# Performance work log

Measured on AMD Instinct MI355X. Metric: run time of the kernel, lower is better.

## Reference

```python
import jax, jax.numpy as jnp
import numpy as np

N_NODES = 50000
N_EDGES = 800000
N_GRAPHS = 64
IN_C = 64
HID = 64
HEADS = 4
NEG_SLOPE = 0.2
EPS = 1e-16


def setup_inputs() -> dict:
    key = jax.random.key(0)
    ks = jax.random.split(key, 16)
    x = jax.random.normal(ks[0], (N_NODES, IN_C), dtype=jnp.float32)
    edge_index = jax.random.randint(ks[1], (2, N_EDGES), 0, N_NODES, dtype=jnp.int64)
    batch = jnp.sort(jax.random.randint(ks[2], (N_NODES,), 0, N_GRAPHS, dtype=jnp.int64))
    s = 1.0 / np.sqrt(IN_C)
    s2 = 1.0 / np.sqrt(HID * HEADS)
    s3 = 1.0 / np.sqrt(HID)
    return {
        "x": x,
        "edge_index": edge_index,
        "batch": batch,
        # GATv2 layer 1: in 64 -> heads*64 = 256 (concat)
        "Wl1": jax.random.normal(ks[3], (IN_C, HEADS * HID), dtype=jnp.float32) * s,
        "Wr1": jax.random.normal(ks[4], (IN_C, HEADS * HID), dtype=jnp.float32) * s,
        "att1": jax.random.normal(ks[5], (HEADS, HID), dtype=jnp.float32) * s3,
        "b1": jnp.zeros((HEADS * HID,), dtype=jnp.float32),
        # GATv2 layer 2: in 256 -> 1 head * 64
        "Wl2": jax.random.normal(ks[6], (HEADS * HID, HID), dtype=jnp.float32) * s2,
        "Wr2": jax.random.normal(ks[7], (HEADS * HID, HID), dtype=jnp.float32) * s2,
        "att2": jax.random.normal(ks[8], (1, HID), dtype=jnp.float32) * s3,
        "b2": jnp.zeros((HID,), dtype=jnp.float32),
        # MLP head: 64 -> 64 -> 2
        "W3": jax.random.normal(ks[9], (HID, 64), dtype=jnp.float32) * s3,
        "b3": jnp.zeros((64,), dtype=jnp.float32),
        "W4": jax.random.normal(ks[10], (64, 2), dtype=jnp.float32) * (1.0 / 8.0),
        "b4": jnp.zeros((2,), dtype=jnp.float32),
    }


def gatv2_conv(x, src, dst, Wl, Wr, att, bias, heads, out_c, n_nodes):
    # PyG GATv2Conv (eval mode, add_self_loops=False, concat heads):
    # x_l = lin_l(x) used for SOURCE nodes (messages), x_r = lin_r(x) for TARGET nodes.
    xl = (x @ Wl).reshape(n_nodes, heads, out_c)
    xr = (x @ Wr).reshape(n_nodes, heads, out_c)
    e = jax.nn.leaky_relu(xl[src] + xr[dst], NEG_SLOPE)          # [E, H, C]
    logits = jnp.einsum('ehc,hc->eh', e, att)                    # [E, H]
    # numerically stable softmax over incoming edges of each target node
    m = jax.ops.segment_max(logits, dst, num_segments=n_nodes)   # [N, H]
    ex = jnp.exp(logits - m[dst])
    denom = jax.ops.segment_sum(ex, dst, num_segments=n_nodes)   # [N, H]
    alpha = ex / (denom[dst] + EPS)                              # [E, H]
    out = jax.ops.segment_sum(alpha[:, :, None] * xl[src], dst, num_segments=n_nodes)
    return out.reshape(n_nodes, heads * out_c) + bias


def reference(x, edge_index, batch, Wl1, Wr1, att1, b1, Wl2, Wr2, att2, b2, W3, b3, W4, b4):
    src, dst = edge_index[0], edge_index[1]
    n = x.shape[0]
    h = gatv2_conv(x, src, dst, Wl1, Wr1, att1, b1, HEADS, HID, n)
    h = jax.nn.elu(h)
    h = gatv2_conv(h, src, dst, Wl2, Wr2, att2, b2, 1, HID, n)
    h = jax.nn.elu(h)
    # global mean pool over graphs
    sums = jax.ops.segment_sum(h, batch, num_segments=N_GRAPHS)
    cnt = jax.ops.segment_sum(jnp.ones((n,), dtype=h.dtype), batch, num_segments=N_GRAPHS)
    pooled = sums / jnp.maximum(cnt, 1.0)[:, None]
    # MLP head (dropout inactive in eval)
    z = jax.nn.relu(pooled @ W3 + b3)
    return z @ W4 + b4
```

## Files before the change

### kernel.cpp

```cpp
#include <hip/hip_runtime.h>
#include <hip/hip_fp16.h>
#include <math.h>

#define N_NODES 50000
#define N_EDGES 800000
#define N_GRAPHS 64
#define L2E 1.44269504f

#if __has_builtin(__builtin_amdgcn_fdot2)
#define HAS_FDOT2 1
typedef _Float16 h2_t __attribute__((ext_vector_type(2)));
#else
#define HAS_FDOT2 0
#endif

typedef _Float16 f16x8 __attribute__((ext_vector_type(8)));
typedef float f32x4 __attribute__((ext_vector_type(4)));

__device__ __forceinline__ float elu1(float v){ return v > 0.f ? v : expm1f(v); }

__device__ __forceinline__ float pkdot(float4 q, const __half2* r2,
        const __half2* A6, const __half2* A4){
    const __half2* qh = (const __half2*)&q;
    float p = 0.f;
#if HAS_FDOT2
    #pragma unroll
    for (int i=0;i<4;i++){
        __half2 u = __hadd2(qh[i], r2[i]);
        __half2 ua = __builtin_bit_cast(__half2,
            __builtin_bit_cast(unsigned, u) & 0x7FFF7FFFu);
        p = __builtin_amdgcn_fdot2(__builtin_bit_cast(h2_t,u),
                                   __builtin_bit_cast(h2_t,A6[i]), p, false);
        p = __builtin_amdgcn_fdot2(__builtin_bit_cast(h2_t,ua),
                                   __builtin_bit_cast(h2_t,A4[i]), p, false);
    }
#else
    #pragma unroll
    for (int i=0;i<4;i++){
        float2 qf = __half22float2(qh[i]);
        float2 rf = __half22float2(r2[i]);
        float2 s6 = __half22float2(A6[i]);
        float2 s4 = __half22float2(A4[i]);
        float u0 = qf.x + rf.x, u1 = qf.y + rf.y;
        p = fmaf(s6.x, u0, fmaf(s4.x, fabsf(u0), p));
        p = fmaf(s6.y, u1, fmaf(s4.y, fabsf(u1), p));
    }
#endif
    return p;
}

__global__ __launch_bounds__(256) void k_prep(const float* __restrict__ x,
        const float* __restrict__ Wl1, const float* __restrict__ Wr1,
        const float* __restrict__ Wl2, const float* __restrict__ Wr2,
        const int* __restrict__ ei,
        __half* __restrict__ xh, __half* __restrict__ Wt1, __half* __restrict__ Wt2,
        int* __restrict__ deg, float* __restrict__ pooled){
    int t = threadIdx.x, bk = blockIdx.x;
    if (bk < 3125){
        int idx = bk*256 + t;
        float4 v = ((const float4*)x)[idx];
        __half2* dst = (__half2*)xh + (size_t)idx*2;
        dst[0] = __floats2half2_rn(v.x, v.y);
        dst[1] = __floats2half2_rn(v.z, v.w);
    } else if (bk < 3381){
        int elem = (bk-3125)*256 + t;
        if (elem < 32768){
            int c = elem >> 6, k = elem & 63;
            float v = (c < 256) ? Wl1[k*256 + c] : Wr1[k*256 + (c-256)];
            Wt1[elem] = __float2half(v);
        } else {
            int e2 = elem - 32768;
            int c = e2 >> 8, k = e2 & 255;
            float v = (c < 64) ? Wl2[k*64 + c] : Wr2[k*64 + (c-64)];
            Wt2[e2] = __float2half(v);
        }
        if (elem < N_GRAPHS*64) pooled[elem] = 0.f;
    } else {
        int e4 = (bk-3381)*256 + t;
        if (e4 < N_EDGES/4){
            int4 d = ((const int4*)(ei + N_EDGES))[e4];
            atomicAdd(&deg[d.x],1); atomicAdd(&deg[d.y],1);
            atomicAdd(&deg[d.z],1); atomicAdd(&deg[d.w],1);
        }
    }
}

__global__ __launch_bounds__(1024) void k_scan_a(const int* __restrict__ deg,
        int* __restrict__ rowptr, int* __restrict__ partial){
    __shared__ int s[1024];
    int t = threadIdx.x; int i = blockIdx.x*1024 + t;
    int v = (i < N_NODES) ? deg[i] : 0;
    s[t] = v; __syncthreads();
    for (int off=1; off<1024; off<<=1){
        int add = (t>=off) ? s[t-off] : 0;
        __syncthreads();
        s[t] += add;
        __syncthreads();
    }
    if (i < N_NODES) rowptr[i] = s[t] - v;
    if (t == 1023) partial[blockIdx.x] = s[1023];
}

__global__ __launch_bounds__(1024) void k_scan_c(int* __restrict__ rowptr,
        int* __restrict__ cursor, const int* __restrict__ partial){
    __shared__ int base;
    if (threadIdx.x == 0){
        int run = 0;
        for (int bk=0; bk<(int)blockIdx.x; bk++) run += partial[bk];
        base = run;
    }
    __syncthreads();
    int i = blockIdx.x*1024 + threadIdx.x;
    if (i < N_NODES){
        int r = rowptr[i] + base;
        rowptr[i] = r; cursor[i] = r;
    } else if (i == N_NODES){
        rowptr[N_NODES] = N_EDGES;
    }
}

__global__ __launch_bounds__(256) void k_mm1(const __half* __restrict__ xh,
        const __half* __restrict__ Wt1,
        __half* __restrict__ xl1h, __half* __restrict__ xr1h,
        const int* __restrict__ ei, int* __restrict__ cursor,
        int* __restrict__ srcs){
    if (blockIdx.y == 4){
        int e4 = blockIdx.x*256 + threadIdx.x;
        if (e4 < N_EDGES/4){
            int4 sv = ((const int4*)ei)[e4];
            int4 dv = ((const int4*)(ei + N_EDGES))[e4];
            int p0 = atomicAdd(&cursor[dv.x],1); srcs[p0] = sv.x;
            int p1 = atomicAdd(&cursor[dv.y],1); srcs[p1] = sv.y;
            int p2 = atomicAdd(&cursor[dv.z],1); srcs[p2] = sv.z;
            int p3 = atomicAdd(&cursor[dv.w],1); srcs[p3] = sv.w;
        }
        return;
    }
    int w = threadIdx.x >> 6, l = threadIdx.x & 63;
    int r0 = blockIdx.x*64 + w*16;
    int cg = blockIdx.y;
    int lr = l & 15, lk = l >> 4, lk4 = lk*4;
    int ar = r0 + lr; if (ar >= N_NODES) ar = N_NODES-1;
    const __half* arow = xh + (size_t)ar*64;
    f16x8 a0 = *(const f16x8*)(arow + lk*8);
    f16x8 a1 = *(const f16x8*)(arow + 32 + lk*8);
    f32x4 acc[8];
    #pragma unroll
    for (int ct=0; ct<8; ct++) acc[ct] = (f32x4){0.f,0.f,0.f,0.f};
    #pragma unroll
    for (int ct=0; ct<8; ct++){
        int col = cg*128 + ct*16 + lr;
        const __half* brow = Wt1 + (size_t)col*64;
        f16x8 b0 = *(const f16x8*)(brow + lk*8);
        f16x8 b1 = *(const f16x8*)(brow + 32 + lk*8);
        acc[ct] = __builtin_amdgcn_mfma_f32_16x16x32_f16(a0, b0, acc[ct], 0,0,0);
        acc[ct] = __builtin_amdgcn_mfma_f32_16x16x32_f16(a1, b1, acc[ct], 0,0,0);
    }
    __half* base = (cg < 2) ? xl1h : xr1h;
    int cbase = (cg < 2) ? cg*128 : (cg-2)*128;
    #pragma unroll
    for (int ct=0; ct<8; ct++){
        int cc = cbase + ct*16 + lr;
        #pragma unroll
        for (int i=0;i<4;i++){
            int row = r0 + lk4 + i;
            if (row < N_NODES) base[(size_t)row*256 + cc] = __float2half(acc[ct][i]);
        }
    }
}

__global__ __launch_bounds__(256) void k_mm2(const __half* __restrict__ h1h,
        const __half* __restrict__ Wt2,
        __half* __restrict__ xl2h, __half* __restrict__ xr2h){
    int w = threadIdx.x >> 6, l = threadIdx.x & 63;
    int r0 = blockIdx.x*64 + w*16;
    int cg = blockIdx.y;
    int lr = l & 15, lk = l >> 4, lk4 = lk*4;
    int ar = r0 + lr; if (ar >= N_NODES) ar = N_NODES-1;
    const __half* arow = h1h + (size_t)ar*256;
    f32x4 acc[4];
    #pragma unroll
    for (int ct=0; ct<4; ct++) acc[ct] = (f32x4){0.f,0.f,0.f,0.f};
    #pragma unroll
    for (int ks=0; ks<8; ks++){
        f16x8 a = *(const f16x8*)(arow + ks*32 + lk*8);
        #pragma unroll
        for (int ct=0; ct<4; ct++){
            int col = cg*64 + ct*16 + lr;
            f16x8 bf = *(const f16x8*)(Wt2 + (size_t)col*256 + ks*32 + lk*8);
            acc[ct] = __builtin_amdgcn_mfma_f32_16x16x32_f16(a, bf, acc[ct], 0,0,0);
        }
    }
    __half* base = (cg == 0) ? xl2h : xr2h;
    #pragma unroll
    for (int ct=0; ct<4; ct++){
        int cc = ct*16 + lr;
        #pragma unroll
        for (int i=0;i<4;i++){
            int row = r0 + lk4 + i;
            if (row < N_NODES) base[(size_t)row*64 + cc] = __float2half(acc[ct][i]);
        }
    }
}

__global__ __launch_bounds__(256) void k_gat1(const __half* __restrict__ xlh,
        const __half* __restrict__ xrh, const int* __restrict__ srcs,
        const int* __restrict__ rowptr, const float* __restrict__ att,
        const float* __restrict__ b, __half* __restrict__ h1h){
    int w = threadIdx.x >> 6, l = threadIdx.x & 63;
    int n = blockIdx.x*4 + w;
    int g = l >> 5, sub = l & 31;
    const float4* xh4 = (const float4*)xlh;
    float4 rq = *(const float4*)(xrh + (size_t)n*256 + sub*8);
    __half2 r2[4];
    { const __half2* rh = (const __half2*)&rq;
      r2[0]=rh[0]; r2[1]=rh[1]; r2[2]=rh[2]; r2[3]=rh[3]; }
    float4 A0v = *(const float4*)(att + sub*8);
    float4 A1v = *(const float4*)(att + sub*8 + 4);
    const float C6 = 0.6f*L2E, C4 = 0.4f*L2E;
    __half2 A6[4] = { __floats2half2_rn(A0v.x*C6, A0v.y*C6),
                      __floats2half2_rn(A0v.z*C6, A0v.w*C6),
                      __floats2half2_rn(A1v.x*C6, A1v.y*C6),
                      __floats2half2_rn(A1v.z*C6, A1v.w*C6) };
    __half2 A4[4] = { __floats2half2_rn(A0v.x*C4, A0v.y*C4),
                      __floats2half2_rn(A0v.z*C4, A0v.w*C4),
                      __floats2half2_rn(A1v.x*C4, A1v.y*C4),
                      __floats2half2_rn(A1v.z*C4, A1v.w*C4) };
    const __half2 Z2 = __floats2half2_rn(0.f, 0.f);
    float accf[8];
    #pragma unroll
    for (int c=0;c<8;c++) accf[c]=0.f;
    float dacc = 0.f;
    int beg = rowptr[n], end = rowptr[n+1];
    for (int j = beg; j < end; j += 8){
        int j0=j+g, j1=j+2+g, j2=j+4+g, j3=j+6+g;
        bool c0=j0<end, c1=j1<end, c2=j2<end, c3=j3<end;
        int s0 = c0 ? srcs[j0] : 0;
        int s1 = c1 ? srcs[j1] : 0;
        int s2 = c2 ? srcs[j2] : 0;
        int s3 = c3 ? srcs[j3] : 0;
        float4 q0 = xh4[(size_t)(unsigned)s0*32 + sub];
        float4 q1 = xh4[(size_t)(unsigned)s1*32 + sub];
        float4 q2 = xh4[(size_t)(unsigned)s2*32 + sub];
        float4 q3 = xh4[(size_t)(unsigned)s3*32 + sub];
        float p0 = pkdot(q0, r2, A6, A4);
        float p1 = pkdot(q1, r2, A6, A4);
        float p2 = pkdot(q2, r2, A6, A4);
        float p3 = pkdot(q3, r2, A6, A4);
        #pragma unroll
        for (int off=1; off<8; off<<=1){
            p0 += __shfl_xor(p0, off);
            p1 += __shfl_xor(p1, off);
            p2 += __shfl_xor(p2, off);
            p3 += __shfl_xor(p3, off);
        }
        float e0 = c0 ? exp2f(p0) : 0.f;
        float e1 = c1 ? exp2f(p1) : 0.f;
        float e2 = c2 ? exp2f(p2) : 0.f;
        float e3 = c3 ? exp2f(p3) : 0.f;
        __half2 E0 = __half2half2(__float2half_rn(e0));
        __half2 E1 = __half2half2(__float2half_rn(e1));
        __half2 E2 = __half2half2(__float2half_rn(e2));
        __half2 E3 = __half2half2(__float2half_rn(e3));
        const __half2* q0h = (const __half2*)&q0;
        const __half2* q1h = (const __half2*)&q1;
        const __half2* q2h = (const __half2*)&q2;
        const __half2* q3h = (const __half2*)&q3;
        #pragma unroll
        for (int i=0;i<4;i++){
            __half2 a16 = __hfma2(E0, q0h[i], Z2);
            a16 = __hfma2(E1, q1h[i], a16);
            a16 = __hfma2(E2, q2h[i], a16);
            a16 = __hfma2(E3, q3h[i], a16);
            float2 f = __half22float2(a16);
            accf[2*i]   += f.x;
            accf[2*i+1] += f.y;
        }
        dacc += e0 + e1 + e2 + e3;
    }
    #pragma unroll
    for (int c=0;c<8;c++) accf[c] += __shfl_xor(accf[c], 32);
    dacc += __shfl_xor(dacc, 32);
    if (l < 32){
        float inv = 1.f / (dacc + 1e-16f);
        float4 B0 = *(const float4*)(b + l*8);
        float4 B1 = *(const float4*)(b + l*8 + 4);
        float4 st;
        __half2* sp = (__half2*)&st;
        sp[0] = __floats2half2_rn(elu1(fmaf(accf[0],inv,B0.x)), elu1(fmaf(accf[1],inv,B0.y)));
        sp[1] = __floats2half2_rn(elu1(fmaf(accf[2],inv,B0.z)), elu1(fmaf(accf[3],inv,B0.w)));
        sp[2] = __floats2half2_rn(elu1(fmaf(accf[4],inv,B1.x)), elu1(fmaf(accf[5],inv,B1.y)));
        sp[3] = __floats2half2_rn(elu1(fmaf(accf[6],inv,B1.z)), elu1(fmaf(accf[7],inv,B1.w)));
        *(float4*)(h1h + (size_t)n*256 + l*8) = st;
    }
}

__global__ __launch_bounds__(256) void k_gat2(const __half* __restrict__ xlh,
        const __half* __restrict__ xrh, const int* __restrict__ srcs,
        const int* __restrict__ rowptr, const float* __restrict__ att,
        const float* __restrict__ b, float* __restrict__ h2){
    int w = threadIdx.x >> 6, l = threadIdx.x & 63;
    int n = blockIdx.x*4 + w;
    int g = l >> 3, sub = l & 7;
    const float4* xh4 = (const float4*)xlh;
    float4 rq = *(const float4*)(xrh + (size_t)n*64 + sub*8);
    __half2 r2[4];
    { const __half2* rh = (const __half2*)&rq;
      r2[0]=rh[0]; r2[1]=rh[1]; r2[2]=rh[2]; r2[3]=rh[3]; }
    float4 A0v = *(const float4*)(att + sub*8);
    float4 A1v = *(const float4*)(att + sub*8 + 4);
    const float C6 = 0.6f*L2E, C4 = 0.4f*L2E;
    __half2 A6[4] = { __floats2half2_rn(A0v.x*C6, A0v.y*C6),
                      __floats2half2_rn(A0v.z*C6, A0v.w*C6),
                      __floats2half2_rn(A1v.x*C6, A1v.y*C6),
                      __floats2half2_rn(A1v.z*C6, A1v.w*C6) };
    __half2 A4[4] = { __floats2half2_rn(A0v.x*C4, A0v.y*C4),
                      __floats2half2_rn(A0v.z*C4, A0v.w*C4),
                      __floats2half2_rn(A1v.x*C4, A1v.y*C4),
                      __floats2half2_rn(A1v.z*C4, A1v.w*C4) };
    const __half2 Z2 = __floats2half2_rn(0.f, 0.f);
    __half2 a16[4] = {Z2, Z2, Z2, Z2};
    float dacc = 0.f;
    int beg = rowptr[n], end = rowptr[n+1];
    for (int j = beg; j < end; j += 16){
        int j0 = j+g, j1 = j+8+g;
        bool c0 = j0<end, c1 = j1<end;
        int s0 = c0 ? srcs[j0] : 0;
        int s1 = c1 ? srcs[j1] : 0;
        float4 q0 = xh4[(size_t)(unsigned)s0*8 + sub];
        float4 q1 = xh4[(size_t)(unsigned)s1*8 + sub];
        float p0 = pkdot(q0, r2, A6, A4);
        float p1 = pkdot(q1, r2, A6, A4);
        #pragma unroll
        for (int off=1; off<8; off<<=1){
            p0 += __shfl_xor(p0, off);
            p1 += __shfl_xor(p1, off);
        }
        float e0 = c0 ? exp2f(p0) : 0.f;
        float e1 = c1 ? exp2f(p1) : 0.f;
        __half2 E0 = __half2half2(__float2half_rn(e0));
        __half2 E1 = __half2half2(__float2half_rn(e1));
        const __half2* q0h = (const __half2*)&q0;
        const __half2* q1h = (const __half2*)&q1;
        #pragma unroll
        for (int i=0;i<4;i++){
            a16[i] = __hfma2(E0, q0h[i], a16[i]);
            a16[i] = __hfma2(E1, q1h[i], a16[i]);
        }
        dacc += e0 + e1;
    }
    float accf[8];
    #pragma unroll
    for (int i=0;i<4;i++){
        float2 f = __half22float2(a16[i]);
        accf[2*i] = f.x; accf[2*i+1] = f.y;
    }
    #pragma unroll
    for (int off=8; off<64; off<<=1){
        #pragma unroll
        for (int c=0;c<8;c++) accf[c] += __shfl_xor(accf[c], off);
        dacc += __shfl_xor(dacc, off);
    }
    if (l < 8){
        float inv = 1.f / (dacc + 1e-16f);
        float4 B0 = *(const float4*)(b + l*8);
        float4 B1 = *(const float4*)(b + l*8 + 4);
        float4 o0, o1;
        o0.x = elu1(fmaf(accf[0], inv, B0.x));
        o0.y = elu1(fmaf(accf[1], inv, B0.y));
        o0.z = elu1(fmaf(accf[2], inv, B0.z));
        o0.w = elu1(fmaf(accf[3], inv, B0.w));
        o1.x = elu1(fmaf(accf[4], inv, B1.x));
        o1.y = elu1(fmaf(accf[5], inv, B1.y));
        o1.z = elu1(fmaf(accf[6], inv, B1.z));
        o1.w = elu1(fmaf(accf[7], inv, B1.w));
        float4* op = (float4*)(h2 + (size_t)n*64 + l*8);
        op[0] = o0; op[1] = o1;
    }
}

__device__ __forceinline__ int lower_bound_i(const int* a, int n, int key){
    int lo = 0, hi = n;
    while (lo < hi){ int mid = (lo+hi)>>1; if (a[mid] < key) lo = mid+1; else hi = mid; }
    return lo;
}

__global__ __launch_bounds__(256) void k_pool(const float* __restrict__ h2,
        const int* __restrict__ batch, float* __restrict__ pooled){
    int gph = blockIdx.x, part = blockIdx.y;
    int t = threadIdx.x, c = t & 63, q = t >> 6;
    int start = lower_bound_i(batch, N_NODES, gph);
    int end   = lower_bound_i(batch, N_NODES, gph+1);
    int len = end - start;
    int is = start + (int)(((long long)len*part) >> 3);
    int ie = start + (int)(((long long)len*(part+1)) >> 3);
    float s = 0.f;
    for (int i = is + q; i < ie; i += 4) s += h2[(size_t)i*64 + c];
    __shared__ float red[256];
    red[t] = s; __syncthreads();
    if (q == 0){
        float tot = red[c] + red[64+c] + red[128+c] + red[192+c];
        atomicAdd(&pooled[gph*64 + c], tot);
    }
}

__global__ __launch_bounds__(64) void k_mlp(const float* __restrict__ pooled,
        const int* __restrict__ batch,
        const float* __restrict__ W3, const float* __restrict__ b3,
        const float* __restrict__ W4, const float* __restrict__ b4,
        float* __restrict__ out){
    int gph = blockIdx.x, t = threadIdx.x;
    __shared__ float ps[64], zs[64];
    int start = lower_bound_i(batch, N_NODES, gph);
    int end   = lower_bound_i(batch, N_NODES, gph+1);
    float cnt = fmaxf((float)(end - start), 1.f);
    ps[t] = pooled[gph*64 + t] / cnt;
    __syncthreads();
    float a = b3[t];
    for (int k=0;k<64;k++) a = fmaf(ps[k], W3[k*64+t], a);
    zs[t] = fmaxf(a, 0.f); __syncthreads();
    if (t < 2){
        float o = b4[t];
        for (int k=0;k<64;k++) o = fmaf(zs[k], W4[k*2+t], o);
        out[gph*2 + t] = o;
    }
}

extern "C" void kernel_launch(void* const* d_in, const int* in_sizes, int n_in,
                              void* d_out, int out_size, void* d_ws, size_t ws_size,
                              hipStream_t stream) {
    const float* x    = (const float*)d_in[0];
    const int*   ei   = (const int*)  d_in[1];
    const int*   batch= (const int*)  d_in[2];
    const float* Wl1  = (const float*)d_in[3];
    const float* Wr1  = (const float*)d_in[4];
    const float* att1 = (const float*)d_in[5];
    const float* b1   = (const float*)d_in[6];
    const float* Wl2  = (const float*)d_in[7];
    const float* Wr2  = (const float*)d_in[8];
    const float* att2 = (const float*)d_in[9];
    const float* b2   = (const float*)d_in[10];
    const float* W3   = (const float*)d_in[11];
    const float* b3   = (const float*)d_in[12];
    const float* W4   = (const float*)d_in[13];
    const float* b4   = (const float*)d_in[14];
    float* out = (float*)d_out;

    char* wsp = (char*)d_ws;
    size_t off = 0;
    auto alloc = [&](size_t bytes) -> char* {
        char* p = wsp + off; off += (bytes + 255) & ~(size_t)255; return p;
    };
    __half* xh    = (__half*)alloc((size_t)N_NODES*64*2);
    __half* Wt1   = (__half*)alloc(512*64*2);
    __half* Wt2   = (__half*)alloc(128*256*2);
    __half* xl1h  = (__half*)alloc((size_t)N_NODES*256*2);
    __half* xr1h  = (__half*)alloc((size_t)N_NODES*256*2);
    __half* h1h   = (__half*)alloc((size_t)N_NODES*256*2);
    int* rowptr   = (int*)alloc((N_NODES+1)*4);
    int* cursor   = (int*)alloc(N_NODES*4);
    int* partial  = (int*)alloc(64*4);
    int* srcs     = (int*)alloc((size_t)N_EDGES*4);
    int* deg      = (int*)alloc(N_NODES*4);
    float* pooled = (float*)alloc(N_GRAPHS*64*4);
    __half* xl2h  = xl1h;
    __half* xr2h  = xl1h + (size_t)N_NODES*64;
    float*  h2    = (float*)xr1h;

    hipMemsetAsync(deg, 0, (size_t)N_NODES*sizeof(int), stream);
    k_prep<<<3125+256+782, 256, 0, stream>>>(x, Wl1, Wr1, Wl2, Wr2, ei,
                                             xh, Wt1, Wt2, deg, pooled);
    k_scan_a<<<49, 1024, 0, stream>>>(deg, rowptr, partial);
    k_scan_c<<<49, 1024, 0, stream>>>(rowptr, cursor, partial);

    k_mm1<<<dim3(782,5), 256, 0, stream>>>(xh, Wt1, xl1h, xr1h, ei, cursor, srcs);
    k_gat1<<<N_NODES/4, 256, 0, stream>>>(xl1h, xr1h, srcs, rowptr, att1, b1, h1h);
    k_mm2<<<dim3(782,2), 256, 0, stream>>>(h1h, Wt2, xl2h, xr2h);
    k_gat2<<<N_NODES/4, 256, 0, stream>>>(xl2h, xr2h, srcs, rowptr, att2, b2, h2);
    k_pool<<<dim3(N_GRAPHS,8), 256, 0, stream>>>(h2, batch, pooled);
    k_mlp<<<N_GRAPHS, 64, 0, stream>>>(pooled, batch, W3, b3, W4, b4, out);
}
```

Before: 293.0 us.

## Stage MFMA outputs through LDS for vectorized stores; split edge scatter into own kernel

The GEMM kernels k_mm1 and k_mm2 now write their MFMA accumulator tiles into per-wave shared memory and then issue 16-byte row-contiguous global stores. This replaces scattered 2-byte half stores and is meant to cut uncoalesced write traffic. The CSR edge scatter that rode along as an extra grid row of k_mm1 is moved into a separate k_scatter launch. That simplifies the GEMM kernel but adds a launch and serializes the scatter with the GEMM instead of overlapping them.

Result: no change. 294.7 us (+0.6%).

```diff
diff --git a/kernel.cpp b/kernel.cpp
--- a/kernel.cpp
+++ b/kernel.cpp
@@ -119,23 +119,23 @@
     }
 }
 
+__global__ void k_scatter(const int* __restrict__ ei, int* __restrict__ cursor,
+                          int* __restrict__ srcs){
+    int e4 = blockIdx.x*256 + threadIdx.x;
+    if (e4 < N_EDGES/4){
+        int4 sv = ((const int4*)ei)[e4];
+        int4 dv = ((const int4*)(ei + N_EDGES))[e4];
+        int p0 = atomicAdd(&cursor[dv.x],1); srcs[p0] = sv.x;
+        int p1 = atomicAdd(&cursor[dv.y],1); srcs[p1] = sv.y;
+        int p2 = atomicAdd(&cursor[dv.z],1); srcs[p2] = sv.z;
+        int p3 = atomicAdd(&cursor[dv.w],1); srcs[p3] = sv.w;
+    }
+}
+
 __global__ __launch_bounds__(256) void k_mm1(const __half* __restrict__ xh,
         const __half* __restrict__ Wt1,
-        __half* __restrict__ xl1h, __half* __restrict__ xr1h,
-        const int* __restrict__ ei, int* __restrict__ cursor,
-        int* __restrict__ srcs){
-    if (blockIdx.y == 4){
-        int e4 = blockIdx.x*256 + threadIdx.x;
-        if (e4 < N_EDGES/4){
-            int4 sv = ((const int4*)ei)[e4];
-            int4 dv = ((const int4*)(ei + N_EDGES))[e4];
-            int p0 = atomicAdd(&cursor[dv.x],1); srcs[p0] = sv.x;
-            int p1 = atomicAdd(&cursor[dv.y],1); srcs[p1] = sv.y;
-            int p2 = atomicAdd(&cursor[dv.z],1); srcs[p2] = sv.z;
-            int p3 = atomicAdd(&cursor[dv.w],1); srcs[p3] = sv.w;
-        }
-        return;
-    }
+        __half* __restrict__ xl1h, __half* __restrict__ xr1h){
+    __shared__ __half lds[4][16*136];
     int w = threadIdx.x >> 6, l = threadIdx.x & 63;
     int r0 = blockIdx.x*64 + w*16;
     int cg = blockIdx.y;
@@ -156,22 +156,28 @@
         acc[ct] = __builtin_amdgcn_mfma_f32_16x16x32_f16(a0, b0, acc[ct], 0,0,0);
         acc[ct] = __builtin_amdgcn_mfma_f32_16x16x32_f16(a1, b1, acc[ct], 0,0,0);
     }
+    #pragma unroll
+    for (int ct=0; ct<8; ct++){
+        #pragma unroll
+        for (int i=0;i<4;i++)
+            lds[w][(lk4+i)*136 + ct*16 + lr] = __float2half(acc[ct][i]);
+    }
     __half* base = (cg < 2) ? xl1h : xr1h;
-    int cbase = (cg < 2) ? cg*128 : (cg-2)*128;
-    #pragma unroll
-    for (int ct=0; ct<8; ct++){
-        int cc = cbase + ct*16 + lr;
-        #pragma unroll
-        for (int i=0;i<4;i++){
-            int row = r0 + lk4 + i;
-            if (row < N_NODES) base[(size_t)row*256 + cc] = __float2half(acc[ct][i]);
-        }
+    int cbase = (cg & 1)*128;
+    #pragma unroll
+    for (int rr=0; rr<4; rr++){
+        int row = rr*4 + lk;
+        float4 v = *(const float4*)&lds[w][row*136 + lr*8];
+        int grow = r0 + row;
+        if (grow < N_NODES)
+            *(float4*)&base[(size_t)grow*256 + cbase + lr*8] = v;
     }
 }
 
 __global__ __launch_bounds__(256) void k_mm2(const __half* __restrict__ h1h,
         const __half* __restrict__ Wt2,
         __half* __restrict__ xl2h, __half* __restrict__ xr2h){
+    __shared__ __half lds[4][16*72];
     int w = threadIdx.x >> 6, l = threadIdx.x & 63;
     int r0 = blockIdx.x*64 + w*16;
     int cg = blockIdx.y;
@@ -191,15 +197,20 @@
             acc[ct] = __builtin_amdgcn_mfma_f32_16x16x32_f16(a, bf, acc[ct], 0,0,0);
         }
     }
+    #pragma unroll
+    for (int ct=0; ct<4; ct++){
+        #pragma unroll
+        for (int i=0;i<4;i++)
+            lds[w][(lk4+i)*72 + ct*16 + lr] = __float2half(acc[ct][i]);
+    }
     __half* base = (cg == 0) ? xl2h : xr2h;
     #pragma unroll
-    for (int ct=0; ct<4; ct++){
-        int cc = ct*16 + lr;
-        #pragma unroll
-        for (int i=0;i<4;i++){
-            int row = r0 + lk4 + i;
-            if (row < N_NODES) base[(size_t)row*64 + cc] = __float2half(acc[ct][i]);
-        }
+    for (int rr=0; rr<2; rr++){
+        int row = rr*8 + (l>>3);
+        float4 v = *(const float4*)&lds[w][row*72 + (l&7)*8];
+        int grow = r0 + row;
+        if (grow < N_NODES)
+            *(float4*)&base[(size_t)grow*64 + (l&7)*8] = v;
     }
 }
 
@@ -472,8 +483,9 @@
                                              xh, Wt1, Wt2, deg, pooled);
     k_scan_a<<<49, 1024, 0, stream>>>(deg, rowptr, partial);
     k_scan_c<<<49, 1024, 0, stream>>>(rowptr, cursor, partial);
-
-    k_mm1<<<dim3(782,5), 256, 0, stream>>>(xh, Wt1, xl1h, xr1h, ei, cursor, srcs);
+    k_scatter<<<782, 256, 0, stream>>>(ei, cursor, srcs);
+
+    k_mm1<<<dim3(782,4), 256, 0, stream>>>(xh, Wt1, xl1h, xr1h);
     k_gat1<<<N_NODES/4, 256, 0, stream>>>(xl1h, xr1h, srcs, rowptr, att1, b1, h1h);
     k_mm2<<<dim3(782,2), 256, 0, stream>>>(h1h, Wt2, xl2h, xr2h);
     k_gat2<<<N_NODES/4, 256, 0, stream>>>(xl2h, xr2h, srcs, rowptr, att2, b2, h2);
```
